# Kernel tuning notes

Hardware: AMD Instinct MI355X
Metric: run time of the kernel (lower is better)

Reference implementation:

```python
import jax, jax.numpy as jnp
import numpy as np

B, S, D, H = 2, 2048, 1024, 16
DK = D // H


def setup_inputs() -> dict:
    key = jax.random.key(0)
    ks = jax.random.split(key, 11)
    s = 1.0 / np.sqrt(D)
    inp = {
        "q": jax.random.normal(ks[0], (B, S, D), jnp.float32),
        "k": jax.random.normal(ks[1], (B, S, D), jnp.float32),
        "v": jax.random.normal(ks[2], (B, S, D), jnp.float32),
        # causal (lower-triangular) decoder mask, broadcast over batch & heads
        "mask": jnp.tril(jnp.ones((S, S), jnp.int32))[None, None, :, :],
        "Wq": jax.random.normal(ks[3], (D, D), jnp.float32) * s,
        "bq": jax.random.normal(ks[4], (D,), jnp.float32) * s,
        "Wk": jax.random.normal(ks[5], (D, D), jnp.float32) * s,
        "bk": jax.random.normal(ks[6], (D,), jnp.float32) * s,
        "Wv": jax.random.normal(ks[7], (D, D), jnp.float32) * s,
        "bv": jax.random.normal(ks[8], (D,), jnp.float32) * s,
        "Wo": jax.random.normal(ks[9], (D, D), jnp.float32) * s,
        "bo": jax.random.normal(ks[10], (D,), jnp.float32) * s,
    }
    return inp


def reference(q, k, v, mask, Wq, bq, Wk, bk, Wv, bv, Wo, bo):
    # projections (nn.Linear: x @ W.T + b)
    def proj(x, W, b):
        return (x @ W.T + b).reshape(B, S, H, DK).transpose(0, 2, 1, 3)  # [B,H,S,DK]

    Q = proj(q, Wq, bq)
    K = proj(k, Wk, bk)
    V = proj(v, Wv, bv)

    scores = jnp.einsum("bhsd,bhtd->bhst", Q, K) / jnp.sqrt(jnp.float32(DK))
    scores = jnp.where(mask == 0, jnp.float32(-1e9), scores)
    attn = jax.nn.softmax(scores, axis=-1)  # dropout=0.0 -> identity
    ctx = jnp.einsum("bhst,bhtd->bhsd", attn, V)
    ctx = ctx.transpose(0, 2, 1, 3).reshape(B, S, D)
    return ctx @ Wo.T + bo
```

## Files before the change

### kernel.cpp

```cpp
#include <hip/hip_runtime.h>

typedef __bf16 bf16;
typedef __bf16 bf16x8 __attribute__((ext_vector_type(8)));
typedef float floatx4 __attribute__((ext_vector_type(4)));

#define NB 2
#define NS 2048
#define ND 1024
#define NH 16
#define NDK 64
#define NM (NB * NS)

__device__ __forceinline__ void async_cp16(const void* g, void* l) {
  __builtin_amdgcn_global_load_lds(
      (const __attribute__((address_space(1))) void*)g,
      (__attribute__((address_space(3))) void*)l, 16, 0, 0);
}

__device__ __forceinline__ bf16x8 cvt8(const float* p) {
  float4 lo = *(const float4*)p, hi = *(const float4*)(p + 4);
  bf16x8 o;
  o[0] = (bf16)lo.x; o[1] = (bf16)lo.y; o[2] = (bf16)lo.z; o[3] = (bf16)lo.w;
  o[4] = (bf16)hi.x; o[5] = (bf16)hi.y; o[6] = (bf16)hi.z; o[7] = (bf16)hi.w;
  return o;
}

struct CvtArgs {
  const float* src[8];
  bf16* dst[8];
  int nblk[8];
  int nseg;
};

__global__ __launch_bounds__(256) void cvt_kernel(CvtArgs a) {
  int b = blockIdx.x, seg = 0;
  while (seg < a.nseg - 1 && b >= a.nblk[seg]) { b -= a.nblk[seg]; ++seg; }
  const size_t idx = ((size_t)b * 256 + threadIdx.x) * 8;
  *(bf16x8*)(a.dst[seg] + idx) = cvt8(a.src[seg] + idx);
}

template <int TM, typename TA, typename TC>
__global__ __launch_bounds__(256) void gemm_dma(
    const TA* __restrict__ A0, const TA* __restrict__ A1, const TA* __restrict__ A2,
    const bf16* __restrict__ W0, const bf16* __restrict__ W1, const bf16* __restrict__ W2,
    const float* __restrict__ bias0, const float* __restrict__ bias1, const float* __restrict__ bias2,
    TC* __restrict__ C0, TC* __restrict__ C1, TC* __restrict__ C2)
{
  const int z = blockIdx.z;
  const TA* A = (z == 0) ? A0 : (z == 1) ? A1 : A2;
  const bf16* W = (z == 0) ? W0 : (z == 1) ? W1 : W2;
  const float* bias = (z == 0) ? bias0 : (z == 1) ? bias1 : bias2;
  TC* C = (z == 0) ? C0 : (z == 1) ? C1 : C2;

  __shared__ bf16 At[TM * 32];
  __shared__ bf16 Bt[128 * 32];

  const int tid = threadIdx.x;
  const int wave = tid >> 6, lane = tid & 63;
  const int q4 = lane >> 4, l15 = lane & 15;
  const int m0 = blockIdx.y * TM, n0 = blockIdx.x * 128;
  constexpr int WM = TM / 2;
  constexpr int MI = WM / 16;
  const int wm = (wave >> 1) * WM, wn = (wave & 1) * 64;

  floatx4 acc[MI][4] = {};

  const bf16* Wg = W + (size_t)(n0 + (lane >> 2)) * ND + (lane & 3) * 8;
  const bf16* Ag = nullptr;
  const float* Af = nullptr;
  const int srow = tid >> 2, sk = (tid & 3) * 8;
  if constexpr (sizeof(TA) == 2)
    Ag = (const bf16*)A + (size_t)(m0 + (lane >> 2)) * ND + (lane & 3) * 8;
  else
    Af = (const float*)A + (size_t)(m0 + srow) * ND + sk;

  for (int k0 = 0; k0 < ND; k0 += 32) {
    bf16x8 a0, a1;
    if constexpr (sizeof(TA) == 4) {
      a0 = cvt8(Af + k0);
      if constexpr (TM == 128) a1 = cvt8(Af + (size_t)64 * ND + k0);
    }
    __syncthreads();
#pragma unroll
    for (int c2 = 0; c2 < 2; ++c2) {
      const int c = wave * 2 + c2;
      async_cp16(Wg + (size_t)c * 16 * ND + k0, &Bt[c * 16 * 32]);
    }
    if constexpr (sizeof(TA) == 2) {
#pragma unroll
      for (int c2 = 0; c2 < TM / 64; ++c2) {
        const int c = wave * (TM / 64) + c2;
        async_cp16(Ag + (size_t)c * 16 * ND + k0, &At[c * 16 * 32]);
      }
    } else {
      *(bf16x8*)&At[srow * 32 + sk] = a0;
      if constexpr (TM == 128) *(bf16x8*)&At[(srow + 64) * 32 + sk] = a1;
    }
    __syncthreads();

    bf16x8 af[MI], bfr[4];
#pragma unroll
    for (int i = 0; i < MI; ++i)
      af[i] = *(const bf16x8*)&At[(wm + i * 16 + l15) * 32 + q4 * 8];
#pragma unroll
    for (int j = 0; j < 4; ++j)
      bfr[j] = *(const bf16x8*)&Bt[(wn + j * 16 + l15) * 32 + q4 * 8];
#pragma unroll
    for (int i = 0; i < MI; ++i)
#pragma unroll
      for (int j = 0; j < 4; ++j)
        acc[i][j] = __builtin_amdgcn_mfma_f32_16x16x32_bf16(af[i], bfr[j], acc[i][j], 0, 0, 0);
  }

#pragma unroll
  for (int j = 0; j < 4; ++j) {
    const int col = n0 + wn + j * 16 + l15;
    const float bv = bias[col];
#pragma unroll
    for (int i = 0; i < MI; ++i) {
      const int rowb = m0 + wm + i * 16 + q4 * 4;
#pragma unroll
      for (int r = 0; r < 4; ++r)
        C[(size_t)(rowb + r) * ND + col] = (TC)(acc[i][j][r] + bv);
    }
  }
}

#define LDV 72

__global__ __launch_bounds__(256) void attn_split(
    const bf16* __restrict__ Q, const bf16* __restrict__ K,
    const bf16* __restrict__ V, bf16* __restrict__ Oh0,
    bf16* __restrict__ Oh1, float* __restrict__ Ps)
{
  __shared__ bf16 vt[2][64 * LDV];
  __shared__ bf16 pbuf[4][16 * LDV];

  const int bx = blockIdx.x;
  const int h = blockIdx.y;
  const int b = blockIdx.z & 1, half = blockIdx.z >> 1;
  bf16* Oh = half ? Oh1 : Oh0;
  const int tid = threadIdx.x, wave = tid >> 6, lane = tid & 63;
  const int q4 = lane >> 4, l15 = lane & 15;
  const int sl = lane;
  const int dbase = wave * 8;

  const bf16* kp = K + ((size_t)(b * NS) + l15) * ND + h * NDK + q4 * 8;
  const bf16* vp = V + ((size_t)(b * NS) + sl) * ND + h * NDK + dbase;

  bf16x8 qf[2];
  floatx4 oacc[4];
  float psum[4];
  bf16x8 kA[8], vA[2], kB[8], vB[2];

  auto ldK = [&](int j, bf16x8 (&kk)[8]) {
    const bf16* p = kp + (size_t)j * (64 * ND);
#pragma unroll
    for (int nf = 0; nf < 4; ++nf)
#pragma unroll
      for (int t = 0; t < 2; ++t)
        kk[nf * 2 + t] = *(const bf16x8*)(p + (size_t)nf * 16 * ND + t * 32);
  };
  auto ldV = [&](int j, bf16x8 (&vv)[2]) {
    const bf16* p = vp + (size_t)j * (64 * ND);
    vv[0] = *(const bf16x8*)(p);
    vv[1] = *(const bf16x8*)(p + 32);
  };

  auto body = [&](int j, int iq, int je, bf16x8 (&kc)[8], bf16x8 (&vc)[2],
                  bf16x8 (&kn)[8], bf16x8 (&vn)[2]) {
    const int cur = j & 1;
#pragma unroll
    for (int it = 0; it < 2; ++it)
#pragma unroll
      for (int e = 0; e < 8; ++e)
        vt[cur][(dbase + it * 32 + e) * LDV + sl] = vc[it][e];

    floatx4 sf[4];
#pragma unroll
    for (int nf = 0; nf < 4; ++nf) {
      floatx4 s = {0.f, 0.f, 0.f, 0.f};
      s = __builtin_amdgcn_mfma_f32_16x16x32_bf16(qf[0], kc[nf * 2 + 0], s, 0, 0, 0);
      s = __builtin_amdgcn_mfma_f32_16x16x32_bf16(qf[1], kc[nf * 2 + 1], s, 0, 0, 0);
      sf[nf] = s;
    }

    if (j + 1 < je) { ldK(j + 1, kn); ldV(j + 1, vn); }

    __syncthreads();

    if (j == iq) {
#pragma unroll
      for (int nf = 0; nf < 4; ++nf) {
        const int kc2 = nf * 16 + l15;
#pragma unroll
        for (int r = 0; r < 4; ++r)
          if (kc2 > wave * 16 + q4 * 4 + r) sf[nf][r] = -1e30f;
      }
    }

#pragma unroll
    for (int nf = 0; nf < 4; ++nf)
#pragma unroll
      for (int r = 0; r < 4; ++r) {
        const float pv = exp2f(sf[nf][r]);
        psum[r] += pv;
        pbuf[wave][(q4 * 4 + r) * LDV + nf * 16 + l15] = (bf16)pv;
      }
    __asm__ __volatile__("s_waitcnt lgkmcnt(0)" ::: "memory");

#pragma unroll
    for (int nf = 0; nf < 4; ++nf)
#pragma unroll
      for (int t = 0; t < 2; ++t) {
        bf16x8 pa = *(const bf16x8*)&pbuf[wave][l15 * LDV + t * 32 + q4 * 8];
        bf16x8 vb = *(const bf16x8*)&vt[cur][(nf * 16 + l15) * LDV + t * 32 + q4 * 8];
        oacc[nf] = __builtin_amdgcn_mfma_f32_16x16x32_bf16(pa, vb, oacc[nf], 0, 0, 0);
      }
  };

  for (int ph = 0; ph < 2; ++ph) {
    const int iq = ph ? (31 - bx) : bx;
    const int n = iq + 1;
    const int h0 = (n + 1) >> 1;
    const int js = half ? h0 : 0;
    const int je = half ? n : h0;
    __syncthreads();

    const size_t qrow0 = (size_t)(b * NS + iq * 64 + wave * 16 + l15);
#pragma unroll
    for (int t = 0; t < 2; ++t) {
      bf16x8 tmp = *(const bf16x8*)(Q + qrow0 * ND + h * NDK + t * 32 + q4 * 8);
#pragma unroll
      for (int e = 0; e < 8; ++e) qf[t][e] = (bf16)((float)tmp[e] * 0.180336880f);
    }

#pragma unroll
    for (int nf = 0; nf < 4; ++nf) oacc[nf] = floatx4{0.f, 0.f, 0.f, 0.f};
#pragma unroll
    for (int r = 0; r < 4; ++r) psum[r] = 0.f;

    if (je > js) {
      ldK(js, kA); ldV(js, vA);
      const int cnt = je - js;
      for (int jj = 0; jj < cnt; ++jj) {
        const int j = js + jj;
        if ((jj & 1) == 0) body(j, iq, je, kA, vA, kB, vB);
        else               body(j, iq, je, kB, vB, kA, vA);
      }
    }

#pragma unroll
    for (int r = 0; r < 4; ++r)
#pragma unroll
      for (int off = 1; off < 16; off <<= 1) psum[r] += __shfl_xor(psum[r], off, 16);

#pragma unroll
    for (int nf = 0; nf < 4; ++nf)
#pragma unroll
      for (int r = 0; r < 4; ++r) {
        const int qrow = iq * 64 + wave * 16 + q4 * 4 + r;
        Oh[(size_t)(b * NS + qrow) * ND + h * NDK + nf * 16 + l15] = (bf16)oacc[nf][r];
      }
    if (l15 == 0) {
#pragma unroll
      for (int r = 0; r < 4; ++r) {
        const int qrow = iq * 64 + wave * 16 + q4 * 4 + r;
        Ps[(((size_t)half * NB + b) * NH + h) * NS + qrow] = psum[r];
      }
    }
  }
}

__global__ __launch_bounds__(256) void attn_combine(
    const bf16* __restrict__ Oh0, const bf16* __restrict__ Oh1,
    const float* __restrict__ Ps, bf16* __restrict__ Ob)
{
  const size_t g = (size_t)blockIdx.x * 256 + threadIdx.x;
  const int row = (int)(g >> 7);
  const int col = ((int)g & 127) * 8;
  const int b = row >> 11, srow = row & (NS - 1);
  const int h = col >> 6;
  const float p0 = Ps[(((size_t)0 * NB + b) * NH + h) * NS + srow];
  const float p1 = Ps[(((size_t)1 * NB + b) * NH + h) * NS + srow];
  const float inv = 1.0f / (p0 + p1);
  const size_t off = (size_t)row * ND + col;
  bf16x8 o0 = *(const bf16x8*)(Oh0 + off);
  bf16x8 o1 = *(const bf16x8*)(Oh1 + off);
  bf16x8 o;
#pragma unroll
  for (int e = 0; e < 8; ++e) o[e] = (bf16)(((float)o0[e] + (float)o1[e]) * inv);
  *(bf16x8*)(Ob + off) = o;
}

__global__ __launch_bounds__(256) void attn_kernel(
    const bf16* __restrict__ Q, const bf16* __restrict__ K,
    const bf16* __restrict__ V, bf16* __restrict__ O)
{
  __shared__ bf16 vt[2][64 * LDV];
  __shared__ bf16 pbuf[4][16 * LDV];

  const int bx = blockIdx.x;
  const int h = blockIdx.y, b = blockIdx.z;
  const int tid = threadIdx.x, wave = tid >> 6, lane = tid & 63;
  const int q4 = lane >> 4, l15 = lane & 15;
  const int sl = lane;
  const int dbase = wave * 8;

  const bf16* kp = K + ((size_t)(b * NS) + l15) * ND + h * NDK + q4 * 8;
  const bf16* vp = V + ((size_t)(b * NS) + sl) * ND + h * NDK + dbase;

  bf16x8 qf[2];
  floatx4 oacc[4];
  float psum[4];
  bf16x8 kA[8], vA[2], kB[8], vB[2];

  auto ldK = [&](int j, bf16x8 (&kk)[8]) {
    const bf16* p = kp + (size_t)j * (64 * ND);
#pragma unroll
    for (int nf = 0; nf < 4; ++nf)
#pragma unroll
      for (int t = 0; t < 2; ++t)
        kk[nf * 2 + t] = *(const bf16x8*)(p + (size_t)nf * 16 * ND + t * 32);
  };
  auto ldV = [&](int j, bf16x8 (&vv)[2]) {
    const bf16* p = vp + (size_t)j * (64 * ND);
    vv[0] = *(const bf16x8*)(p);
    vv[1] = *(const bf16x8*)(p + 32);
  };

  auto body = [&](int j, int iq, bf16x8 (&kc)[8], bf16x8 (&vc)[2],
                  bf16x8 (&kn)[8], bf16x8 (&vn)[2]) {
    const int cur = j & 1;
#pragma unroll
    for (int it = 0; it < 2; ++it)
#pragma unroll
      for (int e = 0; e < 8; ++e)
        vt[cur][(dbase + it * 32 + e) * LDV + sl] = vc[it][e];

    floatx4 sf[4];
#pragma unroll
    for (int nf = 0; nf < 4; ++nf) {
      floatx4 s = {0.f, 0.f, 0.f, 0.f};
      s = __builtin_amdgcn_mfma_f32_16x16x32_bf16(qf[0], kc[nf * 2 + 0], s, 0, 0, 0);
      s = __builtin_amdgcn_mfma_f32_16x16x32_bf16(qf[1], kc[nf * 2 + 1], s, 0, 0, 0);
      sf[nf] = s;
    }

    if (j < iq) { ldK(j + 1, kn); ldV(j + 1, vn); }
    __syncthreads();

    if (j == iq) {
#pragma unroll
      for (int nf = 0; nf < 4; ++nf) {
        const int kc2 = nf * 16 + l15;
#pragma unroll
        for (int r = 0; r < 4; ++r)
          if (kc2 > wave * 16 + q4 * 4 + r) sf[nf][r] = -1e30f;
      }
    }

#pragma unroll
    for (int nf = 0; nf < 4; ++nf)
#pragma unroll
      for (int r = 0; r < 4; ++r) {
        const float pv = exp2f(sf[nf][r]);
        psum[r] += pv;
        pbuf[wave][(q4 * 4 + r) * LDV + nf * 16 + l15] = (bf16)pv;
      }
    __asm__ __volatile__("s_waitcnt lgkmcnt(0)" ::: "memory");

#pragma unroll
    for (int nf = 0; nf < 4; ++nf)
#pragma unroll
      for (int t = 0; t < 2; ++t) {
        bf16x8 pa = *(const bf16x8*)&pbuf[wave][l15 * LDV + t * 32 + q4 * 8];
        bf16x8 vb = *(const bf16x8*)&vt[cur][(nf * 16 + l15) * LDV + t * 32 + q4 * 8];
        oacc[nf] = __builtin_amdgcn_mfma_f32_16x16x32_bf16(pa, vb, oacc[nf], 0, 0, 0);
      }
  };

  for (int ph = 0; ph < 2; ++ph) {
    const int iq = ph ? (31 - bx) : bx;
    __syncthreads();

    const size_t qrow0 = (size_t)(b * NS + iq * 64 + wave * 16 + l15);
#pragma unroll
    for (int t = 0; t < 2; ++t) {
      bf16x8 tmp = *(const bf16x8*)(Q + qrow0 * ND + h * NDK + t * 32 + q4 * 8);
#pragma unroll
      for (int e = 0; e < 8; ++e) qf[t][e] = (bf16)((float)tmp[e] * 0.180336880f);
    }

#pragma unroll
    for (int nf = 0; nf < 4; ++nf) oacc[nf] = floatx4{0.f, 0.f, 0.f, 0.f};
#pragma unroll
    for (int r = 0; r < 4; ++r) psum[r] = 0.f;

    ldK(0, kA); ldV(0, vA);
    for (int j = 0; j <= iq; ++j) {
      if ((j & 1) == 0) body(j, iq, kA, vA, kB, vB);
      else              body(j, iq, kB, vB, kA, vA);
    }

#pragma unroll
    for (int r = 0; r < 4; ++r)
#pragma unroll
      for (int off = 1; off < 16; off <<= 1) psum[r] += __shfl_xor(psum[r], off, 16);

#pragma unroll
    for (int nf = 0; nf < 4; ++nf)
#pragma unroll
      for (int r = 0; r < 4; ++r) {
        const int qrow = iq * 64 + wave * 16 + q4 * 4 + r;
        O[(size_t)(b * NS + qrow) * ND + h * NDK + nf * 16 + l15] =
            (bf16)(oacc[nf][r] / psum[r]);
      }
  }
}

extern "C" void kernel_launch(void* const* d_in, const int* in_sizes, int n_in,
                              void* d_out, int out_size, void* d_ws, size_t ws_size,
                              hipStream_t stream) {
  const float* q  = (const float*)d_in[0];
  const float* k  = (const float*)d_in[1];
  const float* v  = (const float*)d_in[2];
  const float* Wq = (const float*)d_in[4];
  const float* bq = (const float*)d_in[5];
  const float* Wk = (const float*)d_in[6];
  const float* bk = (const float*)d_in[7];
  const float* Wv = (const float*)d_in[8];
  const float* bv = (const float*)d_in[9];
  const float* Wo = (const float*)d_in[10];
  const float* bo = (const float*)d_in[11];
  float* out = (float*)d_out;
  char* w = (char*)d_ws;

  if (ws_size >= (size_t)56 << 20) {
    bf16* xq = (bf16*)(w);
    bf16* xk = (bf16*)(w + ((size_t)8 << 20));
    bf16* xv = (bf16*)(w + ((size_t)16 << 20));
    bf16* wq = (bf16*)(w + ((size_t)24 << 20));
    bf16* wk = (bf16*)(w + ((size_t)26 << 20));
    bf16* wv = (bf16*)(w + ((size_t)28 << 20));
    bf16* wo = (bf16*)(w + ((size_t)30 << 20));
    bf16* Qb = (bf16*)(w + ((size_t)32 << 20));
    bf16* Kb = (bf16*)(w + ((size_t)40 << 20));
    bf16* Vb = (bf16*)(w + ((size_t)48 << 20));
    bf16* Oh0 = xk;
    bf16* Oh1 = xv;
    float* Ps = (float*)wq;
    bf16* Ob = xq;

    CvtArgs ca{};
    const int b4 = (int)((size_t)NM * ND / 2048);
    const int b1 = (int)((size_t)ND * ND / 2048);
    ca.src[0] = q;  ca.dst[0] = xq; ca.nblk[0] = b4;
    ca.src[1] = k;  ca.dst[1] = xk; ca.nblk[1] = b4;
    ca.src[2] = v;  ca.dst[2] = xv; ca.nblk[2] = b4;
    ca.src[3] = Wq; ca.dst[3] = wq; ca.nblk[3] = b1;
    ca.src[4] = Wk; ca.dst[4] = wk; ca.nblk[4] = b1;
    ca.src[5] = Wv; ca.dst[5] = wv; ca.nblk[5] = b1;
    ca.src[6] = Wo; ca.dst[6] = wo; ca.nblk[6] = b1;
    ca.nseg = 7;
    cvt_kernel<<<3 * b4 + 4 * b1, 256, 0, stream>>>(ca);

    gemm_dma<128, bf16, bf16><<<dim3(8, 32, 3), 256, 0, stream>>>(
        xq, xk, xv, wq, wk, wv, bq, bk, bv, Qb, Kb, Vb);
    attn_split<<<dim3(16, NH, NB * 2), 256, 0, stream>>>(Qb, Kb, Vb, Oh0, Oh1, Ps);
    attn_combine<<<(int)((size_t)NM * ND / 8 / 256), 256, 0, stream>>>(Oh0, Oh1, Ps, Ob);
    gemm_dma<64, bf16, float><<<dim3(8, 64, 1), 256, 0, stream>>>(
        Ob, Ob, Ob, wo, wo, wo, bo, bo, bo, out, out, out);
  } else if (ws_size >= (size_t)40 << 20) {
    bf16* wq = (bf16*)(w);
    bf16* wk = (bf16*)(w + ((size_t)2 << 20));
    bf16* wv = (bf16*)(w + ((size_t)4 << 20));
    bf16* wo = (bf16*)(w + ((size_t)6 << 20));
    bf16* Qb = (bf16*)(w + ((size_t)8 << 20));
    bf16* Kb = (bf16*)(w + ((size_t)16 << 20));
    bf16* Vb = (bf16*)(w + ((size_t)24 << 20));
    bf16* Ob = (bf16*)(w + ((size_t)32 << 20));

    CvtArgs ca{};
    const int b1 = (int)((size_t)ND * ND / 2048);
    ca.src[0] = Wq; ca.dst[0] = wq; ca.nblk[0] = b1;
    ca.src[1] = Wk; ca.dst[1] = wk; ca.nblk[1] = b1;
    ca.src[2] = Wv; ca.dst[2] = wv; ca.nblk[2] = b1;
    ca.src[3] = Wo; ca.dst[3] = wo; ca.nblk[3] = b1;
    ca.nseg = 4;
    cvt_kernel<<<4 * b1, 256, 0, stream>>>(ca);

    gemm_dma<128, float, bf16><<<dim3(8, 32, 3), 256, 0, stream>>>(
        q, k, v, wq, wk, wv, bq, bk, bv, Qb, Kb, Vb);
    attn_kernel<<<dim3(16, NH, NB), 256, 0, stream>>>(Qb, Kb, Vb, Ob);
    gemm_dma<64, bf16, float><<<dim3(8, 64, 1), 256, 0, stream>>>(
        Ob, Ob, Ob, wo, wo, wo, bo, bo, bo, out, out, out);
  }
}
```

Measured before the change: 276.5 us.

## Write V transposed from projection GEMM and load it directly into registers in attention

The QKV projection GEMM now writes V in a per-head transposed [B,H,DK,S] layout, so the attention kernel can load V fragments from global memory straight into MFMA registers. This removes the per-tile LDS transpose of V, its double buffer and the block-wide barrier in each iteration. It also adds a launch-bounds occupancy hint. In exchange the GEMM epilogue does strided 8-byte stores, and the V loads are no longer prefetched one tile ahead.

Measured after the change: 409.6 us. 1.48x slower.

```diff
diff --git a/kernel.cpp b/kernel.cpp
--- a/kernel.cpp
+++ b/kernel.cpp
@@ -1,6 +1,7 @@
 #include <hip/hip_runtime.h>
 
 typedef __bf16 bf16;
+typedef __bf16 bf16x4 __attribute__((ext_vector_type(4)));
 typedef __bf16 bf16x8 __attribute__((ext_vector_type(8)));
 typedef float floatx4 __attribute__((ext_vector_type(4)));
 
@@ -39,7 +40,7 @@
   *(bf16x8*)(a.dst[seg] + idx) = cvt8(a.src[seg] + idx);
 }
 
-template <int TM, typename TA, typename TC>
+template <int TM, typename TA, typename TC, bool VTRANS = false>
 __global__ __launch_bounds__(256) void gemm_dma(
     const TA* __restrict__ A0, const TA* __restrict__ A1, const TA* __restrict__ A2,
     const bf16* __restrict__ W0, const bf16* __restrict__ W1, const bf16* __restrict__ W2,
@@ -112,28 +113,45 @@
         acc[i][j] = __builtin_amdgcn_mfma_f32_16x16x32_bf16(af[i], bfr[j], acc[i][j], 0, 0, 0);
   }
 
-#pragma unroll
-  for (int j = 0; j < 4; ++j) {
-    const int col = n0 + wn + j * 16 + l15;
-    const float bv = bias[col];
-#pragma unroll
-    for (int i = 0; i < MI; ++i) {
-      const int rowb = m0 + wm + i * 16 + q4 * 4;
-#pragma unroll
-      for (int r = 0; r < 4; ++r)
-        C[(size_t)(rowb + r) * ND + col] = (TC)(acc[i][j][r] + bv);
+  if (VTRANS && z == 2) {
+#pragma unroll
+    for (int j = 0; j < 4; ++j) {
+      const int col = n0 + wn + j * 16 + l15;
+      const int hh = col >> 6, dk = col & 63;
+      const float bv = bias[col];
+#pragma unroll
+      for (int i = 0; i < MI; ++i) {
+        const int rowb = m0 + wm + i * 16 + q4 * 4;
+        const int bidx = rowb >> 11, s0 = rowb & (NS - 1);
+        bf16x4 pk;
+#pragma unroll
+        for (int r = 0; r < 4; ++r) pk[r] = (bf16)(acc[i][j][r] + bv);
+        *(bf16x4*)((bf16*)C + (((size_t)bidx * NH + hh) * NDK + dk) * NS + s0) = pk;
+      }
+    }
+  } else {
+#pragma unroll
+    for (int j = 0; j < 4; ++j) {
+      const int col = n0 + wn + j * 16 + l15;
+      const float bv = bias[col];
+#pragma unroll
+      for (int i = 0; i < MI; ++i) {
+        const int rowb = m0 + wm + i * 16 + q4 * 4;
+#pragma unroll
+        for (int r = 0; r < 4; ++r)
+          C[(size_t)(rowb + r) * ND + col] = (TC)(acc[i][j][r] + bv);
+      }
     }
   }
 }
 
 #define LDV 72
 
-__global__ __launch_bounds__(256) void attn_split(
+__global__ __launch_bounds__(256, 3) void attn_split(
     const bf16* __restrict__ Q, const bf16* __restrict__ K,
-    const bf16* __restrict__ V, bf16* __restrict__ Oh0,
+    const bf16* __restrict__ Vt, bf16* __restrict__ Oh0,
     bf16* __restrict__ Oh1, float* __restrict__ Ps)
 {
-  __shared__ bf16 vt[2][64 * LDV];
   __shared__ bf16 pbuf[4][16 * LDV];
 
   const int bx = blockIdx.x;
@@ -142,16 +160,14 @@
   bf16* Oh = half ? Oh1 : Oh0;
   const int tid = threadIdx.x, wave = tid >> 6, lane = tid & 63;
   const int q4 = lane >> 4, l15 = lane & 15;
-  const int sl = lane;
-  const int dbase = wave * 8;
 
   const bf16* kp = K + ((size_t)(b * NS) + l15) * ND + h * NDK + q4 * 8;
-  const bf16* vp = V + ((size_t)(b * NS) + sl) * ND + h * NDK + dbase;
+  const bf16* vp = Vt + ((size_t)((b * NH + h) * NDK) + l15) * NS + q4 * 8;
 
   bf16x8 qf[2];
   floatx4 oacc[4];
   float psum[4];
-  bf16x8 kA[8], vA[2], kB[8], vB[2];
+  bf16x8 kA[8], kB[8], vr[8];
 
   auto ldK = [&](int j, bf16x8 (&kk)[8]) {
     const bf16* p = kp + (size_t)j * (64 * ND);
@@ -161,20 +177,17 @@
       for (int t = 0; t < 2; ++t)
         kk[nf * 2 + t] = *(const bf16x8*)(p + (size_t)nf * 16 * ND + t * 32);
   };
-  auto ldV = [&](int j, bf16x8 (&vv)[2]) {
-    const bf16* p = vp + (size_t)j * (64 * ND);
-    vv[0] = *(const bf16x8*)(p);
-    vv[1] = *(const bf16x8*)(p + 32);
+  auto ldV = [&](int j) {
+    const bf16* p = vp + j * 64;
+#pragma unroll
+    for (int nf = 0; nf < 4; ++nf)
+#pragma unroll
+      for (int t = 0; t < 2; ++t)
+        vr[nf * 2 + t] = *(const bf16x8*)(p + (size_t)nf * 16 * NS + t * 32);
   };
 
-  auto body = [&](int j, int iq, int je, bf16x8 (&kc)[8], bf16x8 (&vc)[2],
-                  bf16x8 (&kn)[8], bf16x8 (&vn)[2]) {
-    const int cur = j & 1;
-#pragma unroll
-    for (int it = 0; it < 2; ++it)
-#pragma unroll
-      for (int e = 0; e < 8; ++e)
-        vt[cur][(dbase + it * 32 + e) * LDV + sl] = vc[it][e];
+  auto body = [&](int j, int iq, int je, bf16x8 (&kc)[8], bf16x8 (&kn)[8]) {
+    ldV(j);
 
     floatx4 sf[4];
 #pragma unroll
@@ -185,9 +198,7 @@
       sf[nf] = s;
     }
 
-    if (j + 1 < je) { ldK(j + 1, kn); ldV(j + 1, vn); }
-
-    __syncthreads();
+    if (j + 1 < je) ldK(j + 1, kn);
 
     if (j == iq) {
 #pragma unroll
@@ -210,13 +221,12 @@
     __asm__ __volatile__("s_waitcnt lgkmcnt(0)" ::: "memory");
 
 #pragma unroll
-    for (int nf = 0; nf < 4; ++nf)
-#pragma unroll
-      for (int t = 0; t < 2; ++t) {
-        bf16x8 pa = *(const bf16x8*)&pbuf[wave][l15 * LDV + t * 32 + q4 * 8];
-        bf16x8 vb = *(const bf16x8*)&vt[cur][(nf * 16 + l15) * LDV + t * 32 + q4 * 8];
-        oacc[nf] = __builtin_amdgcn_mfma_f32_16x16x32_bf16(pa, vb, oacc[nf], 0, 0, 0);
-      }
+    for (int t = 0; t < 2; ++t) {
+      bf16x8 pa = *(const bf16x8*)&pbuf[wave][l15 * LDV + t * 32 + q4 * 8];
+#pragma unroll
+      for (int nf = 0; nf < 4; ++nf)
+        oacc[nf] = __builtin_amdgcn_mfma_f32_16x16x32_bf16(pa, vr[nf * 2 + t], oacc[nf], 0, 0, 0);
+    }
   };
 
   for (int ph = 0; ph < 2; ++ph) {
@@ -225,7 +235,6 @@
     const int h0 = (n + 1) >> 1;
     const int js = half ? h0 : 0;
     const int je = half ? n : h0;
-    __syncthreads();
 
     const size_t qrow0 = (size_t)(b * NS + iq * 64 + wave * 16 + l15);
 #pragma unroll
@@ -241,12 +250,12 @@
     for (int r = 0; r < 4; ++r) psum[r] = 0.f;
 
     if (je > js) {
-      ldK(js, kA); ldV(js, vA);
+      ldK(js, kA);
       const int cnt = je - js;
       for (int jj = 0; jj < cnt; ++jj) {
         const int j = js + jj;
-        if ((jj & 1) == 0) body(j, iq, je, kA, vA, kB, vB);
-        else               body(j, iq, je, kB, vB, kA, vA);
+        if ((jj & 1) == 0) body(j, iq, je, kA, kB);
+        else               body(j, iq, je, kB, kA);
       }
     }
 
@@ -446,7 +455,7 @@
     bf16* wo = (bf16*)(w + ((size_t)30 << 20));
     bf16* Qb = (bf16*)(w + ((size_t)32 << 20));
     bf16* Kb = (bf16*)(w + ((size_t)40 << 20));
-    bf16* Vb = (bf16*)(w + ((size_t)48 << 20));
+    bf16* Vt = (bf16*)(w + ((size_t)48 << 20));
     bf16* Oh0 = xk;
     bf16* Oh1 = xv;
     float* Ps = (float*)wq;
@@ -465,9 +474,9 @@
     ca.nseg = 7;
     cvt_kernel<<<3 * b4 + 4 * b1, 256, 0, stream>>>(ca);
 
-    gemm_dma<128, bf16, bf16><<<dim3(8, 32, 3), 256, 0, stream>>>(
-        xq, xk, xv, wq, wk, wv, bq, bk, bv, Qb, Kb, Vb);
-    attn_split<<<dim3(16, NH, NB * 2), 256, 0, stream>>>(Qb, Kb, Vb, Oh0, Oh1, Ps);
+    gemm_dma<128, bf16, bf16, true><<<dim3(8, 32, 3), 256, 0, stream>>>(
+        xq, xk, xv, wq, wk, wv, bq, bk, bv, Qb, Kb, Vt);
+    attn_split<<<dim3(16, NH, NB * 2), 256, 0, stream>>>(Qb, Kb, Vt, Oh0, Oh1, Ps);
     attn_combine<<<(int)((size_t)NM * ND / 8 / 256), 256, 0, stream>>>(Oh0, Oh1, Ps, Ob);
     gemm_dma<64, bf16, float><<<dim3(8, 64, 1), 256, 0, stream>>>(
         Ob, Ob, Ob, wo, wo, wo, bo, bo, bo, out, out, out);
```
